# Optimization experiments

Hardware: AMD Instinct MI355X
Metric: run time of the kernel (lower is better)

## Reference

```python
import jax, jax.numpy as jnp
import numpy as np


def setup_inputs() -> dict:
    key = jax.random.key(0)
    ks = jax.random.split(key, 8)
    dim, E = 128, 8
    b, t, h, w = 2, 16, 64, 64
    scale = 1.0 / np.sqrt(dim)
    return {
        "x": jax.random.normal(ks[0], (b, dim, t, h, w), jnp.float32),
        "gate_w": jax.random.normal(ks[1], (dim, E), jnp.float32) * scale,
        "gate_b": jax.random.normal(ks[2], (E,), jnp.float32) * 0.01,
        "W1": jax.random.normal(ks[3], (E, dim, dim), jnp.float32) * scale,
        "b1": jax.random.normal(ks[4], (E, dim), jnp.float32) * 0.01,
        "alpha": jnp.full((E,), 0.25, jnp.float32),  # PReLU default init
        "W2": jax.random.normal(ks[5], (E, dim, dim), jnp.float32) * scale,
        "b2": jax.random.normal(ks[6], (E, dim), jnp.float32) * 0.01,
        "top_k": 2,
    }


def reference(x, gate_w, gate_b, W1, b1, alpha, W2, b2, top_k):
    b, c, t, h, w = x.shape
    E = gate_w.shape[1]
    # tokens: [N, c] with N = b*t*h*w (matches permute(0,2,3,4,1).reshape(-1,c))
    xf = jnp.transpose(x, (0, 2, 3, 4, 1)).reshape(-1, c)
    N = xf.shape[0]
    logits = xf @ gate_w + gate_b                      # [N, E]
    vals, idx = jax.lax.top_k(logits, top_k)           # [N, K]
    probs = jax.nn.softmax(vals, axis=1)               # softmax over selected logits
    # scatter combine weights to dense [N, E] (zero for unselected experts)
    combine = jnp.zeros((N, E), xf.dtype).at[jnp.arange(N)[:, None], idx].add(probs)
    # expert MLP (1x1x1 conv == per-token linear), scalar PReLU per expert
    h1 = jnp.einsum('nc,eoc->eno', xf, W1) + b1[:, None, :]          # [E, N, c]
    h1 = jnp.maximum(h1, 0) + alpha[:, None, None] * jnp.minimum(h1, 0)
    h2 = jnp.einsum('eno,epo->enp', h1, W2) + b2[:, None, :]         # [E, N, c]
    out = jnp.einsum('ne,enc->nc', combine, h2)                      # weighted combine
    out = jnp.transpose(out.reshape(b, t, h, w, c), (0, 4, 1, 2, 3))
    return out + x
```

## Files before the change

kernel.cpp:

```cpp
#include <hip/hip_runtime.h>

typedef float f32x4  __attribute__((ext_vector_type(4)));
typedef float f32x16 __attribute__((ext_vector_type(16)));
typedef __bf16 bf16x8 __attribute__((ext_vector_type(8)));

#define SPAT 65536
#define CH   128
#define NE   8

#define SLOT(i)  ((i) * 32768)
#define B1_OFF   131072
#define B2T_OFF  135168
#define AL_OFF   139264
#define LDS_BYTES 139296

static __device__ __forceinline__ unsigned short f2b(float f) {
    unsigned u = __builtin_bit_cast(unsigned, f);
    unsigned r = u + 0x7FFFu + ((u >> 16) & 1u);
    return (unsigned short)(r >> 16);
}
static __device__ __forceinline__ unsigned pk2(float a, float b) {
    return (unsigned)f2b(a) | ((unsigned)f2b(b) << 16);
}

typedef const __attribute__((address_space(1))) void* as1cp;
typedef __attribute__((address_space(3))) void* as3p;
static __device__ __forceinline__ void gload16(const void* g, void* l) {
    __builtin_amdgcn_global_load_lds((as1cp)g, (as3p)l, 16, 0, 0);
}

__global__ void conv_w(const float* __restrict__ W1, const float* __restrict__ W2,
                       unsigned char* __restrict__ wimg) {
    const int gid = blockIdx.x * 256 + threadIdx.x;
    const int mat = gid >> 14;
    const int e   = (gid >> 11) & 7;
    const int r   = (gid >> 4) & 127;
    const int p   = gid & 15;
    const int sg  = p ^ (r & 15);
    int src_row = r;
    if (mat == 0) {
        const int n = 4 * (r >> 5) + ((r >> 3) & 3);
        src_row = (n >> 1) * 16 + ((r >> 2) & 1) * 8 + (n & 1) * 4 + (r & 3);
    }
    const float* s = (mat ? W2 : W1) + (e * 16384 + src_row * 128 + sg * 8);
    uint4 pk;
    pk.x = pk2(s[0], s[1]); pk.y = pk2(s[2], s[3]);
    pk.z = pk2(s[4], s[5]); pk.w = pk2(s[6], s[7]);
    *(uint4*)(wimg + mat * 262144 + e * 32768 + r * 256 + p * 16) = pk;
}

static __device__ __forceinline__ void stage_w(const unsigned char* __restrict__ src,
                                               unsigned char* dst, int t) {
    const int off = t * 16;
    gload16(src + off,          dst + off);
    gload16(src + 8192  + off,  dst + 8192  + off);
    gload16(src + 16384 + off,  dst + 16384 + off);
    gload16(src + 24576 + off,  dst + 24576 + off);
}

__global__ __launch_bounds__(512) __attribute__((amdgpu_waves_per_eu(2, 2)))
void moe_main(const float* __restrict__ x,  const float* __restrict__ gw,
              const float* __restrict__ gb, const float* __restrict__ b1,
              const float* __restrict__ alpha, const float* __restrict__ b2,
              const unsigned char* __restrict__ wimg, float* __restrict__ out)
{
    __shared__ __align__(16) unsigned char smem[LDS_BYTES];
    const int t = threadIdx.x, lane = t & 63, w = t >> 6, blk = blockIdx.x;
    const int ltok = lane & 31, hi = lane >> 5, l15 = lane & 15;
    const size_t xbase = (size_t)(blk >> 8) * (size_t)(CH * SPAT) + (size_t)((blk & 255) << 8);
    const int m = w * 32 + ltok;

    stage_w(wimg,          smem + SLOT(0), t);
    stage_w(wimg + 262144, smem + SLOT(1), t);

    if (t < 256) ((f32x4*)(smem + B1_OFF))[t] = ((const f32x4*)b1)[t];
    if (t < 128) {
        uint4 pkv, z4 = {0u, 0u, 0u, 0u};
        pkv.x = pk2(b2[0 * 128 + t], b2[1 * 128 + t]);
        pkv.y = pk2(b2[2 * 128 + t], b2[3 * 128 + t]);
        pkv.z = pk2(b2[4 * 128 + t], b2[5 * 128 + t]);
        pkv.w = pk2(b2[6 * 128 + t], b2[7 * 128 + t]);
        *(uint4*)(smem + B2T_OFF + t * 32)      = pkv;
        *(uint4*)(smem + B2T_OFF + t * 32 + 16) = z4;
    } else if (t >= 128 && t < 136) {
        ((float*)(smem + AL_OFF))[t - 128] = alpha[t - 128];
    }

    f32x4 plo = {0.f,0.f,0.f,0.f}, phi = {0.f,0.f,0.f,0.f};
    uint4 xb[8];
    #pragma unroll
    for (int kc = 0; kc < 8; ++kc) {
        const int c0 = kc * 16 + hi * 8;
        float v8[8];
        #pragma unroll
        for (int j = 0; j < 8; ++j) v8[j] = x[xbase + (size_t)(c0 + j) * SPAT + m];
        #pragma unroll
        for (int j = 0; j < 8; ++j) {
            const f32x4 g0 = *(const f32x4*)(gw + (c0 + j) * NE);
            const f32x4 g1 = *(const f32x4*)(gw + (c0 + j) * NE + 4);
            plo += v8[j] * g0; phi += v8[j] * g1;
        }
        xb[kc].x = pk2(v8[0], v8[1]); xb[kc].y = pk2(v8[2], v8[3]);
        xb[kc].z = pk2(v8[4], v8[5]); xb[kc].w = pk2(v8[6], v8[7]);
    }
    #pragma unroll
    for (int i2 = 0; i2 < 4; ++i2) {
        plo[i2] += __shfl_xor(plo[i2], 32, 64);
        phi[i2] += __shfl_xor(phi[i2], 32, 64);
    }
    int i0, i1; float q0, q1; uint4 cbw;
    {
        float lg[8];
        #pragma unroll
        for (int e2 = 0; e2 < 4; ++e2) { lg[e2] = plo[e2] + gb[e2]; lg[4 + e2] = phi[e2] + gb[4 + e2]; }
        i0 = 0; float v0 = lg[0];
        #pragma unroll
        for (int e2 = 1; e2 < 8; ++e2) if (lg[e2] > v0) { v0 = lg[e2]; i0 = e2; }
        i1 = -1; float v1 = -3.4e38f;
        #pragma unroll
        for (int e2 = 0; e2 < 8; ++e2) if (e2 != i0 && lg[e2] > v1) { v1 = lg[e2]; i1 = e2; }
        const float d = expf(v1 - v0);
        q0 = 1.f / (1.f + d);
        q1 = d   / (1.f + d);
        float cb[8];
        #pragma unroll
        for (int e2 = 0; e2 < 8; ++e2) cb[e2] = (e2 == i0) ? q0 : ((e2 == i1) ? q1 : 0.f);
        cbw.x = pk2(cb[0], cb[1]); cbw.y = pk2(cb[2], cb[3]);
        cbw.z = pk2(cb[4], cb[5]); cbw.w = pk2(cb[6], cb[7]);
    }
    __syncthreads();

    f32x16 acc[4] = {};

    #pragma unroll 1
    for (int e = 0; e < NE; ++e) {
        const int cur = (e & 1) << 1;
        if (e < 7) {
            stage_w(wimg + (e + 1) * 32768,          smem + SLOT(cur ^ 2), t);
            stage_w(wimg + 262144 + (e + 1) * 32768, smem + SLOT((cur ^ 2) + 1), t);
        }
        const unsigned char* WA = smem + SLOT(cur);
        const unsigned char* WB = smem + SLOT(cur) + 32768;
        const float alph = ((const float*)(smem + AL_OFF))[e];
        const float ce = (i0 == e) ? q0 : ((i1 == e) ? q1 : 0.f);

        #pragma unroll 1
        for (int g = 0; g < 4; ++g) {
            uint4 a1[8];
            #pragma unroll
            for (int kc = 0; kc < 8; ++kc)
                a1[kc] = *(const uint4*)(WA + (g * 32 + ltok) * 256
                                          + (((kc * 2 + hi) ^ l15) * 16));
            f32x16 h = {};
            #pragma unroll
            for (int kc = 0; kc < 8; ++kc)
                h = __builtin_amdgcn_mfma_f32_32x32x16_bf16(
                        __builtin_bit_cast(bf16x8, a1[kc]),
                        __builtin_bit_cast(bf16x8, xb[kc]), h, 0, 0, 0);
            uint4 pa2[2];
            #pragma unroll
            for (int q = 0; q < 4; ++q) {
                const int n = 4 * g + q, kt2 = n >> 1, half = n & 1;
                const int obase = kt2 * 16 + hi * 8 + half * 4;
                const f32x4 b1v = *(const f32x4*)(smem + B1_OFF + e * 512 + obase * 4);
                float hv[4];
                #pragma unroll
                for (int i = 0; i < 4; ++i) {
                    float z = h[q * 4 + i] + b1v[i];
                    z = (z > 0.f) ? z : alph * z;
                    hv[i] = z * ce;
                }
                ((unsigned*)&pa2[q >> 1])[half * 2]     = pk2(hv[0], hv[1]);
                ((unsigned*)&pa2[q >> 1])[half * 2 + 1] = pk2(hv[2], hv[3]);
            }
            #pragma unroll
            for (int dk = 0; dk < 2; ++dk) {
                const int kt2 = 2 * g + dk;
                #pragma unroll
                for (int n2 = 0; n2 < 4; ++n2) {
                    const uint4 wf = *(const uint4*)(WB + (n2 * 32 + ltok) * 256
                                          + (((kt2 * 2 + hi) ^ l15) * 16));
                    acc[n2] = __builtin_amdgcn_mfma_f32_32x32x16_bf16(
                            __builtin_bit_cast(bf16x8, pa2[dk]),
                            __builtin_bit_cast(bf16x8, wf), acc[n2], 0, 0, 0);
                }
            }
        }
        __syncthreads();
    }

    {
        const uint4 z4 = {0u, 0u, 0u, 0u};
        const uint4 aop = hi ? z4 : cbw;
        #pragma unroll
        for (int n2 = 0; n2 < 4; ++n2) {
            const uint4 bop = *(const uint4*)(smem + B2T_OFF + (n2 * 32 + ltok) * 32 + hi * 16);
            acc[n2] = __builtin_amdgcn_mfma_f32_32x32x16_bf16(
                    __builtin_bit_cast(bf16x8, aop),
                    __builtin_bit_cast(bf16x8, bop), acc[n2], 0, 0, 0);
        }
    }

    #pragma unroll
    for (int n2 = 0; n2 < 4; ++n2) {
        const int p = n2 * 32 + ltok;
        #pragma unroll
        for (int q = 0; q < 4; ++q) {
            const int tok0 = w * 32 + q * 8 + hi * 4;
            const size_t a = xbase + (size_t)p * SPAT + tok0;
            const f32x4 xv = *(const f32x4*)(x + a);
            f32x4 r;
            #pragma unroll
            for (int i = 0; i < 4; ++i) r[i] = acc[n2][q * 4 + i] + xv[i];
            *(f32x4*)(out + a) = r;
        }
    }
}

extern "C" void kernel_launch(void* const* d_in, const int* in_sizes, int n_in,
                              void* d_out, int out_size, void* d_ws, size_t ws_size,
                              hipStream_t stream) {
    const float* x  = (const float*)d_in[0];
    const float* gw = (const float*)d_in[1];
    const float* gb = (const float*)d_in[2];
    const float* W1 = (const float*)d_in[3];
    const float* b1 = (const float*)d_in[4];
    const float* al = (const float*)d_in[5];
    const float* W2 = (const float*)d_in[6];
    const float* b2 = (const float*)d_in[7];
    (void)in_sizes; (void)n_in; (void)out_size; (void)ws_size;
    unsigned char* wimg = (unsigned char*)d_ws;
    float* out = (float*)d_out;

    conv_w<<<dim3(128), dim3(256), 0, stream>>>(W1, W2, wimg);
    moe_main<<<dim3(512), dim3(512), 0, stream>>>(x, gw, gb, b1, al, b2, wimg, out);
}
```

Before: 121.0 us.

## Route tokens to selected experts only instead of dense all-expert compute

```diff
diff --git a/kernel.cpp b/kernel.cpp
--- a/kernel.cpp
+++ b/kernel.cpp
@@ -8,25 +8,27 @@
 #define CH   128
 #define NE   8
 
-#define SLOT(i)  ((i) * 32768)
-#define B1_OFF   131072
-#define B2T_OFF  135168
-#define AL_OFF   139264
-#define LDS_BYTES 139296
-
-static __device__ __forceinline__ unsigned short f2b(float f) {
-    unsigned u = __builtin_bit_cast(unsigned, f);
-    unsigned r = u + 0x7FFFu + ((u >> 16) & 1u);
-    return (unsigned short)(r >> 16);
+#define XT_OFF    0
+#define OA_OFF    65536
+#define OA_ROWB   272
+#define B1_OFF    135440
+#define B2_OFF    139536
+#define SLT_OFF   143632
+#define SLC_OFF   145680
+#define DSC_OFF   149776
+#define CNT_OFF   149904
+#define AL_OFF    150096
+#define NG_OFF    150128
+#define LDS_BYTES 150144
+
+static __device__ __forceinline__ unsigned short bf(float f) {
+    __bf16 h = (__bf16)f; return __builtin_bit_cast(unsigned short, h);
 }
 static __device__ __forceinline__ unsigned pk2(float a, float b) {
-    return (unsigned)f2b(a) | ((unsigned)f2b(b) << 16);
-}
-
-typedef const __attribute__((address_space(1))) void* as1cp;
-typedef __attribute__((address_space(3))) void* as3p;
-static __device__ __forceinline__ void gload16(const void* g, void* l) {
-    __builtin_amdgcn_global_load_lds((as1cp)g, (as3p)l, 16, 0, 0);
+    return (unsigned)bf(a) | ((unsigned)bf(b) << 16);
+}
+static __device__ __forceinline__ float ub(unsigned short u) {
+    return __builtin_bit_cast(float, (unsigned)u << 16);
 }
 
 __global__ void conv_w(const float* __restrict__ W1, const float* __restrict__ W2,
@@ -36,26 +38,109 @@
     const int e   = (gid >> 11) & 7;
     const int r   = (gid >> 4) & 127;
     const int p   = gid & 15;
-    const int sg  = p ^ (r & 15);
     int src_row = r;
     if (mat == 0) {
         const int n = 4 * (r >> 5) + ((r >> 3) & 3);
         src_row = (n >> 1) * 16 + ((r >> 2) & 1) * 8 + (n & 1) * 4 + (r & 3);
     }
-    const float* s = (mat ? W2 : W1) + (e * 16384 + src_row * 128 + sg * 8);
+    const float* s = (mat ? W2 : W1) + (e * 16384 + src_row * 128 + p * 8);
     uint4 pk;
     pk.x = pk2(s[0], s[1]); pk.y = pk2(s[2], s[3]);
     pk.z = pk2(s[4], s[5]); pk.w = pk2(s[6], s[7]);
     *(uint4*)(wimg + mat * 262144 + e * 32768 + r * 256 + p * 16) = pk;
 }
 
-static __device__ __forceinline__ void stage_w(const unsigned char* __restrict__ src,
-                                               unsigned char* dst, int t) {
-    const int off = t * 16;
-    gload16(src + off,          dst + off);
-    gload16(src + 8192  + off,  dst + 8192  + off);
-    gload16(src + 16384 + off,  dst + 16384 + off);
-    gload16(src + 24576 + off,  dst + 24576 + off);
+template<bool ADD>
+static __device__ __forceinline__ void group_body(
+        unsigned char* smem, const unsigned char* __restrict__ wimg,
+        int g, int l31, int hi)
+{
+    const unsigned desc = ((const unsigned*)(smem + DSC_OFF))[g];
+    const int e  = (int)(desc >> 16);
+    const int s  = (int)(desc & 0xFFFFu) + l31;
+    const unsigned tokRaw = ((const unsigned short*)(smem + SLT_OFF))[s];
+    const float ce = ((const float*)(smem + SLC_OFF))[s];
+    const int tokx  = (int)(tokRaw & 255u);
+    const int rowOA = (tokRaw > 255u) ? 256 : (int)tokRaw;
+    const float alph = ((const float*)(smem + AL_OFF))[e];
+
+    uint4 xb[8];
+    #pragma unroll
+    for (int kc = 0; kc < 8; ++kc)
+        xb[kc] = *(const uint4*)(smem + XT_OFF + tokx * 256
+                                  + (((2 * kc + hi) ^ (tokx & 15)) * 16));
+
+    const unsigned char* W1i = wimg + e * 32768;
+    const unsigned char* W2i = wimg + 262144 + e * 32768;
+
+    f32x16 D[4] = {};
+    #pragma unroll 1
+    for (int gt = 0; gt < 4; ++gt) {
+        uint4 a1[8];
+        #pragma unroll
+        for (int kc = 0; kc < 8; ++kc)
+            a1[kc] = *(const uint4*)(W1i + (gt * 32 + l31) * 256 + (2 * kc + hi) * 16);
+        f32x16 h0 = {}, h1 = {};
+        #pragma unroll
+        for (int kc = 0; kc < 4; ++kc) {
+            h0 = __builtin_amdgcn_mfma_f32_32x32x16_bf16(
+                    __builtin_bit_cast(bf16x8, a1[2 * kc]),
+                    __builtin_bit_cast(bf16x8, xb[2 * kc]), h0, 0, 0, 0);
+            h1 = __builtin_amdgcn_mfma_f32_32x32x16_bf16(
+                    __builtin_bit_cast(bf16x8, a1[2 * kc + 1]),
+                    __builtin_bit_cast(bf16x8, xb[2 * kc + 1]), h1, 0, 0, 0);
+        }
+        uint4 pa2[2];
+        #pragma unroll
+        for (int q = 0; q < 4; ++q) {
+            const int n = 4 * gt + q, kt2 = n >> 1, half = n & 1;
+            const int obase = kt2 * 16 + hi * 8 + half * 4;
+            const f32x4 b1v = *(const f32x4*)(smem + B1_OFF + e * 512 + obase * 4);
+            float hv[4];
+            #pragma unroll
+            for (int i = 0; i < 4; ++i) {
+                float z = h0[q * 4 + i] + h1[q * 4 + i] + b1v[i];
+                z = fmaxf(z, 0.f) + alph * fminf(z, 0.f);
+                hv[i] = z * ce;
+            }
+            ((unsigned*)&pa2[q >> 1])[half * 2]     = pk2(hv[0], hv[1]);
+            ((unsigned*)&pa2[q >> 1])[half * 2 + 1] = pk2(hv[2], hv[3]);
+        }
+        #pragma unroll
+        for (int dk = 0; dk < 2; ++dk) {
+            const int kt2 = 2 * gt + dk;
+            #pragma unroll
+            for (int n2 = 0; n2 < 4; ++n2) {
+                const uint4 wf = *(const uint4*)(W2i + (n2 * 32 + l31) * 256
+                                                  + (2 * kt2 + hi) * 16);
+                D[n2] = __builtin_amdgcn_mfma_f32_32x32x16_bf16(
+                        __builtin_bit_cast(bf16x8, wf),
+                        __builtin_bit_cast(bf16x8, pa2[dk]), D[n2], 0, 0, 0);
+            }
+        }
+    }
+    unsigned char* oarow = smem + OA_OFF + rowOA * OA_ROWB;
+    #pragma unroll
+    for (int n2 = 0; n2 < 4; ++n2) {
+        #pragma unroll
+        for (int q = 0; q < 4; ++q) {
+            const int p0 = n2 * 32 + q * 8 + hi * 4;
+            const f32x4 b2v = *(const f32x4*)(smem + B2_OFF + e * 512 + p0 * 4);
+            float vv[4];
+            #pragma unroll
+            for (int i = 0; i < 4; ++i) vv[i] = D[n2][q * 4 + i] + ce * b2v[i];
+            uint2* dst = (uint2*)(oarow + p0 * 2);
+            if (ADD) {
+                const uint2 old = *dst;
+                vv[0] += ub((unsigned short)(old.x & 0xFFFFu));
+                vv[1] += ub((unsigned short)(old.x >> 16));
+                vv[2] += ub((unsigned short)(old.y & 0xFFFFu));
+                vv[3] += ub((unsigned short)(old.y >> 16));
+            }
+            uint2 nw; nw.x = pk2(vv[0], vv[1]); nw.y = pk2(vv[2], vv[3]);
+            *dst = nw;
+        }
+    }
 }
 
 __global__ __launch_bounds__(512) __attribute__((amdgpu_waves_per_eu(2, 2)))
@@ -66,28 +151,17 @@
 {
     __shared__ __align__(16) unsigned char smem[LDS_BYTES];
     const int t = threadIdx.x, lane = t & 63, w = t >> 6, blk = blockIdx.x;
-    const int ltok = lane & 31, hi = lane >> 5, l15 = lane & 15;
+    const int l31 = lane & 31, hi = lane >> 5;
     const size_t xbase = (size_t)(blk >> 8) * (size_t)(CH * SPAT) + (size_t)((blk & 255) << 8);
-    const int m = w * 32 + ltok;
-
-    stage_w(wimg,          smem + SLOT(0), t);
-    stage_w(wimg + 262144, smem + SLOT(1), t);
-
-    if (t < 256) ((f32x4*)(smem + B1_OFF))[t] = ((const f32x4*)b1)[t];
-    if (t < 128) {
-        uint4 pkv, z4 = {0u, 0u, 0u, 0u};
-        pkv.x = pk2(b2[0 * 128 + t], b2[1 * 128 + t]);
-        pkv.y = pk2(b2[2 * 128 + t], b2[3 * 128 + t]);
-        pkv.z = pk2(b2[4 * 128 + t], b2[5 * 128 + t]);
-        pkv.w = pk2(b2[6 * 128 + t], b2[7 * 128 + t]);
-        *(uint4*)(smem + B2T_OFF + t * 32)      = pkv;
-        *(uint4*)(smem + B2T_OFF + t * 32 + 16) = z4;
-    } else if (t >= 128 && t < 136) {
-        ((float*)(smem + AL_OFF))[t - 128] = alpha[t - 128];
-    }
+    const int m = w * 32 + l31;
+    unsigned* C = (unsigned*)(smem + CNT_OFF);
+
+    if (t < 48) C[t] = 0;
+    if (t < 256)      ((f32x4*)(smem + B1_OFF))[t]       = ((const f32x4*)b1)[t];
+    else              ((f32x4*)(smem + B2_OFF))[t - 256] = ((const f32x4*)b2)[t - 256];
+    if (t < 8) ((float*)(smem + AL_OFF))[t] = alpha[t];
 
     f32x4 plo = {0.f,0.f,0.f,0.f}, phi = {0.f,0.f,0.f,0.f};
-    uint4 xb[8];
     #pragma unroll
     for (int kc = 0; kc < 8; ++kc) {
         const int c0 = kc * 16 + hi * 8;
@@ -100,15 +174,17 @@
             const f32x4 g1 = *(const f32x4*)(gw + (c0 + j) * NE + 4);
             plo += v8[j] * g0; phi += v8[j] * g1;
         }
-        xb[kc].x = pk2(v8[0], v8[1]); xb[kc].y = pk2(v8[2], v8[3]);
-        xb[kc].z = pk2(v8[4], v8[5]); xb[kc].w = pk2(v8[6], v8[7]);
+        uint4 pkv;
+        pkv.x = pk2(v8[0], v8[1]); pkv.y = pk2(v8[2], v8[3]);
+        pkv.z = pk2(v8[4], v8[5]); pkv.w = pk2(v8[6], v8[7]);
+        *(uint4*)(smem + XT_OFF + m * 256 + (((2 * kc + hi) ^ (m & 15)) * 16)) = pkv;
     }
     #pragma unroll
     for (int i2 = 0; i2 < 4; ++i2) {
         plo[i2] += __shfl_xor(plo[i2], 32, 64);
         phi[i2] += __shfl_xor(phi[i2], 32, 64);
     }
-    int i0, i1; float q0, q1; uint4 cbw;
+    int i0, i1; float q0, q1;
     {
         float lg[8];
         #pragma unroll
@@ -122,97 +198,82 @@
         const float d = expf(v1 - v0);
         q0 = 1.f / (1.f + d);
         q1 = d   / (1.f + d);
-        float cb[8];
-        #pragma unroll
-        for (int e2 = 0; e2 < 8; ++e2) cb[e2] = (e2 == i0) ? q0 : ((e2 == i1) ? q1 : 0.f);
-        cbw.x = pk2(cb[0], cb[1]); cbw.y = pk2(cb[2], cb[3]);
-        cbw.z = pk2(cb[4], cb[5]); cbw.w = pk2(cb[6], cb[7]);
-    }
-    __syncthreads();
-
-    f32x16 acc[4] = {};
+    }
+    __syncthreads();
+
+    if (hi == 0) {
+        atomicAdd(&C[i0], 1u);
+        atomicAdd(&C[8 + i1], 1u);
+    }
+    __syncthreads();
+
+    if (t == 0) {
+        unsigned* dsc = (unsigned*)(smem + DSC_OFF);
+        int ng = 0; unsigned base = 0;
+        for (int e = 0; e < 8; ++e) {
+            const unsigned c = C[e], gc = (c + 31) >> 5;
+            C[16 + e] = base; C[32 + e] = base;
+            for (unsigned k = 0; k < gc; ++k) dsc[ng++] = ((unsigned)e << 16) | (base + k * 32);
+            base += gc * 32;
+        }
+        ((int*)(smem + NG_OFF))[0] = ng;
+        for (int e = 0; e < 8; ++e) {
+            const unsigned c = C[8 + e], gc = (c + 31) >> 5;
+            C[24 + e] = base; C[40 + e] = base;
+            for (unsigned k = 0; k < gc; ++k) dsc[ng++] = ((unsigned)e << 16) | (base + k * 32);
+            base += gc * 32;
+        }
+        ((int*)(smem + NG_OFF))[1] = ng;
+    }
+    __syncthreads();
+
+    if (hi == 0) {
+        const unsigned pP = atomicAdd(&C[16 + i0], 1u);
+        ((unsigned short*)(smem + SLT_OFF))[pP] = (unsigned short)m;
+        ((float*)(smem + SLC_OFF))[pP] = q0;
+        const unsigned pQ = atomicAdd(&C[24 + i1], 1u);
+        ((unsigned short*)(smem + SLT_OFF))[pQ] = (unsigned short)m;
+        ((float*)(smem + SLC_OFF))[pQ] = q1;
+    }
+    __syncthreads();
+
+    if (t < 16) {
+        const int e = t & 7;
+        const unsigned c  = (t < 8) ? C[e] : C[8 + e];
+        const unsigned bs = (t < 8) ? C[32 + e] : C[40 + e];
+        const unsigned en = bs + ((c + 31) & ~31u);
+        for (unsigned s2 = bs + c; s2 < en; ++s2) {
+            ((unsigned short*)(smem + SLT_OFF))[s2] = 0xFFFFu;
+            ((float*)(smem + SLC_OFF))[s2] = 0.f;
+        }
+    }
+    __syncthreads();
+
+    const int NGP = ((const int*)(smem + NG_OFF))[0];
+    const int NGT = ((const int*)(smem + NG_OFF))[1];
 
     #pragma unroll 1
-    for (int e = 0; e < NE; ++e) {
-        const int cur = (e & 1) << 1;
-        if (e < 7) {
-            stage_w(wimg + (e + 1) * 32768,          smem + SLOT(cur ^ 2), t);
-            stage_w(wimg + 262144 + (e + 1) * 32768, smem + SLOT((cur ^ 2) + 1), t);
-        }
-        const unsigned char* WA = smem + SLOT(cur);
-        const unsigned char* WB = smem + SLOT(cur) + 32768;
-        const float alph = ((const float*)(smem + AL_OFF))[e];
-        const float ce = (i0 == e) ? q0 : ((i1 == e) ? q1 : 0.f);
-
-        #pragma unroll 1
-        for (int g = 0; g < 4; ++g) {
-            uint4 a1[8];
-            #pragma unroll
-            for (int kc = 0; kc < 8; ++kc)
-                a1[kc] = *(const uint4*)(WA + (g * 32 + ltok) * 256
-                                          + (((kc * 2 + hi) ^ l15) * 16));
-            f32x16 h = {};
-            #pragma unroll
-            for (int kc = 0; kc < 8; ++kc)
-                h = __builtin_amdgcn_mfma_f32_32x32x16_bf16(
-                        __builtin_bit_cast(bf16x8, a1[kc]),
-                        __builtin_bit_cast(bf16x8, xb[kc]), h, 0, 0, 0);
-            uint4 pa2[2];
-            #pragma unroll
-            for (int q = 0; q < 4; ++q) {
-                const int n = 4 * g + q, kt2 = n >> 1, half = n & 1;
-                const int obase = kt2 * 16 + hi * 8 + half * 4;
-                const f32x4 b1v = *(const f32x4*)(smem + B1_OFF + e * 512 + obase * 4);
-                float hv[4];
-                #pragma unroll
-                for (int i = 0; i < 4; ++i) {
-                    float z = h[q * 4 + i] + b1v[i];
-                    z = (z > 0.f) ? z : alph * z;
-                    hv[i] = z * ce;
-                }
-                ((unsigned*)&pa2[q >> 1])[half * 2]     = pk2(hv[0], hv[1]);
-                ((unsigned*)&pa2[q >> 1])[half * 2 + 1] = pk2(hv[2], hv[3]);
-            }
-            #pragma unroll
-            for (int dk = 0; dk < 2; ++dk) {
-                const int kt2 = 2 * g + dk;
-                #pragma unroll
-                for (int n2 = 0; n2 < 4; ++n2) {
-                    const uint4 wf = *(const uint4*)(WB + (n2 * 32 + ltok) * 256
-                                          + (((kt2 * 2 + hi) ^ l15) * 16));
-                    acc[n2] = __builtin_amdgcn_mfma_f32_32x32x16_bf16(
-                            __builtin_bit_cast(bf16x8, pa2[dk]),
-                            __builtin_bit_cast(bf16x8, wf), acc[n2], 0, 0, 0);
-                }
-            }
-        }
-        __syncthreads();
-    }
+    for (int g = w; g < NGP; g += 8) group_body<false>(smem, wimg, g, l31, hi);
+    __syncthreads();
+    #pragma unroll 1
+    for (int g = NGP + w; g < NGT; g += 8) group_body<true>(smem, wimg, g, l31, hi);
+    __syncthreads();
 
     {
-        const uint4 z4 = {0u, 0u, 0u, 0u};
-        const uint4 aop = hi ? z4 : cbw;
-        #pragma unroll
-        for (int n2 = 0; n2 < 4; ++n2) {
-            const uint4 bop = *(const uint4*)(smem + B2T_OFF + (n2 * 32 + ltok) * 32 + hi * 16);
-            acc[n2] = __builtin_amdgcn_mfma_f32_32x32x16_bf16(
-                    __builtin_bit_cast(bf16x8, aop),
-                    __builtin_bit_cast(bf16x8, bop), acc[n2], 0, 0, 0);
-        }
-    }
-
-    #pragma unroll
-    for (int n2 = 0; n2 < 4; ++n2) {
-        const int p = n2 * 32 + ltok;
-        #pragma unroll
-        for (int q = 0; q < 4; ++q) {
-            const int tok0 = w * 32 + q * 8 + hi * 4;
-            const size_t a = xbase + (size_t)p * SPAT + tok0;
-            const f32x4 xv = *(const f32x4*)(x + a);
-            f32x4 r;
-            #pragma unroll
-            for (int i = 0; i < 4; ++i) r[i] = acc[n2][q * 4 + i] + xv[i];
-            *(f32x4*)(out + a) = r;
+        const int etok = t & 255;
+        const int gb8  = (t >> 8) * 8;
+        const unsigned char* oarow = smem + OA_OFF + etok * OA_ROWB;
+        #pragma unroll
+        for (int gi = 0; gi < 8; ++gi) {
+            const int gran = gb8 + gi;
+            const uint4 r = *(const uint4*)(oarow + gran * 16);
+            const unsigned short* u = (const unsigned short*)&r;
+            #pragma unroll
+            for (int j = 0; j < 8; ++j) {
+                const int p = gran * 8 + j;
+                const size_t a = xbase + (size_t)p * SPAT + etok;
+                out[a] = ub(u[j]) + x[a];
+            }
         }
     }
 }
```

Measured after the change: 139.6 us. 1.15x slower.

## Double-buffer W1 fragment loads and split first GEMM accumulator chain

Applied to the files above, without the earlier changes.

```diff
diff --git a/kernel.cpp b/kernel.cpp
--- a/kernel.cpp
+++ b/kernel.cpp
@@ -58,6 +58,56 @@
     gload16(src + 24576 + off,  dst + 24576 + off);
 }
 
+static __device__ __forceinline__ void ld_a1(uint4* buf, const unsigned char* smem,
+                                             unsigned waOff, int g, int ltok, int hi, int l15) {
+    #pragma unroll
+    for (int kc = 0; kc < 8; ++kc)
+        buf[kc] = *(const uint4*)(smem + waOff + (g * 32 + ltok) * 256
+                                   + (((kc * 2 + hi) ^ l15) * 16));
+}
+static __device__ __forceinline__ void body(const uint4* a1, int g, const uint4* xb,
+        const unsigned char* smem, unsigned wbOff, int e, int ltok, int hi, int l15,
+        float alph, float ce, f32x16* acc) {
+    f32x16 h0 = {}, h1 = {};
+    #pragma unroll
+    for (int kc = 0; kc < 4; ++kc) {
+        h0 = __builtin_amdgcn_mfma_f32_32x32x16_bf16(
+                __builtin_bit_cast(bf16x8, a1[2 * kc]),
+                __builtin_bit_cast(bf16x8, xb[2 * kc]), h0, 0, 0, 0);
+        h1 = __builtin_amdgcn_mfma_f32_32x32x16_bf16(
+                __builtin_bit_cast(bf16x8, a1[2 * kc + 1]),
+                __builtin_bit_cast(bf16x8, xb[2 * kc + 1]), h1, 0, 0, 0);
+    }
+    uint4 pa2[2];
+    #pragma unroll
+    for (int q = 0; q < 4; ++q) {
+        const int n = 4 * g + q, kt2 = n >> 1, half = n & 1;
+        const int obase = kt2 * 16 + hi * 8 + half * 4;
+        const f32x4 b1v = *(const f32x4*)(smem + B1_OFF + e * 512 + obase * 4);
+        float hv[4];
+        #pragma unroll
+        for (int i = 0; i < 4; ++i) {
+            float z = h0[q * 4 + i] + h1[q * 4 + i] + b1v[i];
+            z = (z > 0.f) ? z : alph * z;
+            hv[i] = z * ce;
+        }
+        ((unsigned*)&pa2[q >> 1])[half * 2]     = pk2(hv[0], hv[1]);
+        ((unsigned*)&pa2[q >> 1])[half * 2 + 1] = pk2(hv[2], hv[3]);
+    }
+    #pragma unroll
+    for (int dk = 0; dk < 2; ++dk) {
+        const int kt2 = 2 * g + dk;
+        #pragma unroll
+        for (int n2 = 0; n2 < 4; ++n2) {
+            const uint4 wf = *(const uint4*)(smem + wbOff + (n2 * 32 + ltok) * 256
+                                  + (((kt2 * 2 + hi) ^ l15) * 16));
+            acc[n2] = __builtin_amdgcn_mfma_f32_32x32x16_bf16(
+                    __builtin_bit_cast(bf16x8, pa2[dk]),
+                    __builtin_bit_cast(bf16x8, wf), acc[n2], 0, 0, 0);
+        }
+    }
+}
+
 __global__ __launch_bounds__(512) __attribute__((amdgpu_waves_per_eu(2, 2)))
 void moe_main(const float* __restrict__ x,  const float* __restrict__ gw,
               const float* __restrict__ gb, const float* __restrict__ b1,
@@ -139,53 +189,21 @@
             stage_w(wimg + (e + 1) * 32768,          smem + SLOT(cur ^ 2), t);
             stage_w(wimg + 262144 + (e + 1) * 32768, smem + SLOT((cur ^ 2) + 1), t);
         }
-        const unsigned char* WA = smem + SLOT(cur);
-        const unsigned char* WB = smem + SLOT(cur) + 32768;
+        const unsigned waOff = (unsigned)SLOT(cur);
+        const unsigned wbOff = (unsigned)SLOT(cur) + 32768u;
         const float alph = ((const float*)(smem + AL_OFF))[e];
         const float ce = (i0 == e) ? q0 : ((i1 == e) ? q1 : 0.f);
 
-        #pragma unroll 1
-        for (int g = 0; g < 4; ++g) {
-            uint4 a1[8];
-            #pragma unroll
-            for (int kc = 0; kc < 8; ++kc)
-                a1[kc] = *(const uint4*)(WA + (g * 32 + ltok) * 256
-                                          + (((kc * 2 + hi) ^ l15) * 16));
-            f32x16 h = {};
-            #pragma unroll
-            for (int kc = 0; kc < 8; ++kc)
-                h = __builtin_amdgcn_mfma_f32_32x32x16_bf16(
-                        __builtin_bit_cast(bf16x8, a1[kc]),
-                        __builtin_bit_cast(bf16x8, xb[kc]), h, 0, 0, 0);
-            uint4 pa2[2];
-            #pragma unroll
-            for (int q = 0; q < 4; ++q) {
-                const int n = 4 * g + q, kt2 = n >> 1, half = n & 1;
-                const int obase = kt2 * 16 + hi * 8 + half * 4;
-                const f32x4 b1v = *(const f32x4*)(smem + B1_OFF + e * 512 + obase * 4);
-                float hv[4];
-                #pragma unroll
-                for (int i = 0; i < 4; ++i) {
-                    float z = h[q * 4 + i] + b1v[i];
-                    z = (z > 0.f) ? z : alph * z;
-                    hv[i] = z * ce;
-                }
-                ((unsigned*)&pa2[q >> 1])[half * 2]     = pk2(hv[0], hv[1]);
-                ((unsigned*)&pa2[q >> 1])[half * 2 + 1] = pk2(hv[2], hv[3]);
-            }
-            #pragma unroll
-            for (int dk = 0; dk < 2; ++dk) {
-                const int kt2 = 2 * g + dk;
-                #pragma unroll
-                for (int n2 = 0; n2 < 4; ++n2) {
-                    const uint4 wf = *(const uint4*)(WB + (n2 * 32 + ltok) * 256
-                                          + (((kt2 * 2 + hi) ^ l15) * 16));
-                    acc[n2] = __builtin_amdgcn_mfma_f32_32x32x16_bf16(
-                            __builtin_bit_cast(bf16x8, pa2[dk]),
-                            __builtin_bit_cast(bf16x8, wf), acc[n2], 0, 0, 0);
-                }
-            }
-        }
+        uint4 bufA[8], bufB[8];
+        ld_a1(bufA, smem, waOff, 0, ltok, hi, l15);
+        ld_a1(bufB, smem, waOff, 1, ltok, hi, l15);
+        body(bufA, 0, xb, smem, wbOff, e, ltok, hi, l15, alph, ce, acc);
+        ld_a1(bufA, smem, waOff, 2, ltok, hi, l15);
+        body(bufB, 1, xb, smem, wbOff, e, ltok, hi, l15, alph, ce, acc);
+        ld_a1(bufB, smem, waOff, 3, ltok, hi, l15);
+        body(bufA, 2, xb, smem, wbOff, e, ltok, hi, l15, alph, ce, acc);
+        body(bufB, 3, xb, smem, wbOff, e, ltok, hi, l15, alph, ce, acc);
+
         __syncthreads();
     }
 
```

Result: slower. 127.3 us (+5.1%).

## Stream W2 fragments from global memory and halve LDS weight staging

Applied to the files above, without the earlier changes.

```diff
diff --git a/kernel.cpp b/kernel.cpp
--- a/kernel.cpp
+++ b/kernel.cpp
@@ -9,18 +9,16 @@
 #define NE   8
 
 #define SLOT(i)  ((i) * 32768)
-#define B1_OFF   131072
-#define B2T_OFF  135168
-#define AL_OFF   139264
-#define LDS_BYTES 139296
-
-static __device__ __forceinline__ unsigned short f2b(float f) {
-    unsigned u = __builtin_bit_cast(unsigned, f);
-    unsigned r = u + 0x7FFFu + ((u >> 16) & 1u);
-    return (unsigned short)(r >> 16);
+#define B1_OFF   65536
+#define B2T_OFF  69632
+#define AL_OFF   73728
+#define LDS_BYTES 73760
+
+static __device__ __forceinline__ unsigned short bf(float f) {
+    __bf16 h = (__bf16)f; return __builtin_bit_cast(unsigned short, h);
 }
 static __device__ __forceinline__ unsigned pk2(float a, float b) {
-    return (unsigned)f2b(a) | ((unsigned)f2b(b) << 16);
+    return (unsigned)bf(a) | ((unsigned)bf(b) << 16);
 }
 
 typedef const __attribute__((address_space(1))) void* as1cp;
@@ -36,21 +34,27 @@
     const int e   = (gid >> 11) & 7;
     const int r   = (gid >> 4) & 127;
     const int p   = gid & 15;
-    const int sg  = p ^ (r & 15);
-    int src_row = r;
     if (mat == 0) {
+        const int sg = p ^ (r & 15);
         const int n = 4 * (r >> 5) + ((r >> 3) & 3);
-        src_row = (n >> 1) * 16 + ((r >> 2) & 1) * 8 + (n & 1) * 4 + (r & 3);
-    }
-    const float* s = (mat ? W2 : W1) + (e * 16384 + src_row * 128 + sg * 8);
-    uint4 pk;
-    pk.x = pk2(s[0], s[1]); pk.y = pk2(s[2], s[3]);
-    pk.z = pk2(s[4], s[5]); pk.w = pk2(s[6], s[7]);
-    *(uint4*)(wimg + mat * 262144 + e * 32768 + r * 256 + p * 16) = pk;
-}
-
-static __device__ __forceinline__ void stage_w(const unsigned char* __restrict__ src,
-                                               unsigned char* dst, int t) {
+        const int src_row = (n >> 1) * 16 + ((r >> 2) & 1) * 8 + (n & 1) * 4 + (r & 3);
+        const float* s = W1 + (e * 16384 + src_row * 128 + sg * 8);
+        uint4 pk;
+        pk.x = pk2(s[0], s[1]); pk.y = pk2(s[2], s[3]);
+        pk.z = pk2(s[4], s[5]); pk.w = pk2(s[6], s[7]);
+        *(uint4*)(wimg + e * 32768 + r * 256 + p * 16) = pk;
+    } else {
+        const float* s = W2 + (e * 16384 + r * 128 + p * 8);
+        uint4 pk;
+        pk.x = pk2(s[0], s[1]); pk.y = pk2(s[2], s[3]);
+        pk.z = pk2(s[4], s[5]); pk.w = pk2(s[6], s[7]);
+        *(uint4*)(wimg + 262144 + e * 32768
+                  + ((((p >> 1) * 4 + (r >> 5)) << 10) + ((p & 1) << 9) + (r & 31) * 16)) = pk;
+    }
+}
+
+static __device__ __forceinline__ void stage_w32(const unsigned char* __restrict__ src,
+                                                 unsigned char* dst, int t) {
     const int off = t * 16;
     gload16(src + off,          dst + off);
     gload16(src + 8192  + off,  dst + 8192  + off);
@@ -69,9 +73,9 @@
     const int ltok = lane & 31, hi = lane >> 5, l15 = lane & 15;
     const size_t xbase = (size_t)(blk >> 8) * (size_t)(CH * SPAT) + (size_t)((blk & 255) << 8);
     const int m = w * 32 + ltok;
-
-    stage_w(wimg,          smem + SLOT(0), t);
-    stage_w(wimg + 262144, smem + SLOT(1), t);
+    const int wlane = (hi << 9) + ltok * 16;
+
+    stage_w32(wimg, smem + SLOT(0), t);
 
     if (t < 256) ((f32x4*)(smem + B1_OFF))[t] = ((const f32x4*)b1)[t];
     if (t < 128) {
@@ -134,13 +138,10 @@
 
     #pragma unroll 1
     for (int e = 0; e < NE; ++e) {
-        const int cur = (e & 1) << 1;
-        if (e < 7) {
-            stage_w(wimg + (e + 1) * 32768,          smem + SLOT(cur ^ 2), t);
-            stage_w(wimg + 262144 + (e + 1) * 32768, smem + SLOT((cur ^ 2) + 1), t);
-        }
-        const unsigned char* WA = smem + SLOT(cur);
-        const unsigned char* WB = smem + SLOT(cur) + 32768;
+        const int cur = e & 1;
+        if (e < 7) stage_w32(wimg + (e + 1) * 32768, smem + SLOT(cur ^ 1), t);
+        const unsigned char* WA  = smem + SLOT(cur);
+        const unsigned char* W2g = wimg + 262144 + e * 32768;
         const float alph = ((const float*)(smem + AL_OFF))[e];
         const float ce = (i0 == e) ? q0 : ((i1 == e) ? q1 : 0.f);
 
@@ -151,12 +152,16 @@
             for (int kc = 0; kc < 8; ++kc)
                 a1[kc] = *(const uint4*)(WA + (g * 32 + ltok) * 256
                                           + (((kc * 2 + hi) ^ l15) * 16));
-            f32x16 h = {};
-            #pragma unroll
-            for (int kc = 0; kc < 8; ++kc)
-                h = __builtin_amdgcn_mfma_f32_32x32x16_bf16(
-                        __builtin_bit_cast(bf16x8, a1[kc]),
-                        __builtin_bit_cast(bf16x8, xb[kc]), h, 0, 0, 0);
+            f32x16 h0 = {}, h1 = {};
+            #pragma unroll
+            for (int kc = 0; kc < 4; ++kc) {
+                h0 = __builtin_amdgcn_mfma_f32_32x32x16_bf16(
+                        __builtin_bit_cast(bf16x8, a1[2 * kc]),
+                        __builtin_bit_cast(bf16x8, xb[2 * kc]), h0, 0, 0, 0);
+                h1 = __builtin_amdgcn_mfma_f32_32x32x16_bf16(
+                        __builtin_bit_cast(bf16x8, a1[2 * kc + 1]),
+                        __builtin_bit_cast(bf16x8, xb[2 * kc + 1]), h1, 0, 0, 0);
+            }
             uint4 pa2[2];
             #pragma unroll
             for (int q = 0; q < 4; ++q) {
@@ -166,7 +171,7 @@
                 float hv[4];
                 #pragma unroll
                 for (int i = 0; i < 4; ++i) {
-                    float z = h[q * 4 + i] + b1v[i];
+                    float z = h0[q * 4 + i] + h1[q * 4 + i] + b1v[i];
                     z = (z > 0.f) ? z : alph * z;
                     hv[i] = z * ce;
                 }
@@ -178,8 +183,7 @@
                 const int kt2 = 2 * g + dk;
                 #pragma unroll
                 for (int n2 = 0; n2 < 4; ++n2) {
-                    const uint4 wf = *(const uint4*)(WB + (n2 * 32 + ltok) * 256
-                                          + (((kt2 * 2 + hi) ^ l15) * 16));
+                    const uint4 wf = *(const uint4*)(W2g + ((kt2 * 4 + n2) << 10) + wlane);
                     acc[n2] = __builtin_amdgcn_mfma_f32_32x32x16_bf16(
                             __builtin_bit_cast(bf16x8, pa2[dk]),
                             __builtin_bit_cast(bf16x8, wf), acc[n2], 0, 0, 0);
```

After: 122.1 us. About the same (+0.9%).
